# Kernel tuning notes

Measured on AMD Instinct MI355X. Metric: run time of the kernel, lower is better.

Reference implementation:

```python
import jax, jax.numpy as jnp
import numpy as np

NF = 64      # num_feat
NFR = 5      # num_frames
G = 8        # offset/deformable groups
CENTER = NFR // 2
K = 9        # 3x3 taps


def conv3x3(x, w, b):
    y = jax.lax.conv_general_dilated(x, w, (1, 1), 'SAME',
                                     dimension_numbers=('NCHW', 'OIHW', 'NCHW'))
    return y + b[None, :, None, None]


def mdcn(x, offsets, masks, w, b):
    # x: [B,C,H,W]; offsets: [B,2*G*K,H,W] (layout g,k,(y,x)); masks: [B,G*K,H,W]
    B, C, H, W = x.shape
    Cg = C // G
    off = offsets.reshape(B, G, K, 2, H, W)
    oy, ox = off[:, :, :, 0], off[:, :, :, 1]          # [B,G,K,H,W]
    m = masks.reshape(B, G, K, H, W)
    ky = jnp.repeat(jnp.arange(3), 3) - 1              # [K]
    kx = jnp.tile(jnp.arange(3), 3) - 1
    base_y = (ky[:, None, None] + jnp.arange(H)[None, :, None]).astype(x.dtype)  # [K,H,1]
    base_x = (kx[:, None, None] + jnp.arange(W)[None, None, :]).astype(x.dtype)  # [K,1,W]
    py = oy + base_y[None, None]                        # [B,G,K,H,W]
    px = ox + base_x[None, None]
    y0f = jnp.floor(py); x0f = jnp.floor(px)
    ty = py - y0f; tx = px - x0f
    y0 = y0f.astype(jnp.int32); x0 = x0f.astype(jnp.int32)
    xg = x.reshape(B, G, Cg, H * W)

    def gather(yi, xi):
        valid = (yi >= 0) & (yi < H) & (xi >= 0) & (xi < W)
        yc = jnp.clip(yi, 0, H - 1); xc = jnp.clip(xi, 0, W - 1)
        idx = (yc * W + xc).reshape(B, G, 1, K * H * W)
        idx = jnp.broadcast_to(idx, (B, G, Cg, K * H * W))
        v = jnp.take_along_axis(xg, idx, axis=3).reshape(B, G, Cg, K, H, W)
        return v * valid.reshape(B, G, 1, K, H, W)

    v00 = gather(y0, x0); v01 = gather(y0, x0 + 1)
    v10 = gather(y0 + 1, x0); v11 = gather(y0 + 1, x0 + 1)
    ty_ = ty[:, :, None]; tx_ = tx[:, :, None]          # [B,G,1,K,H,W]
    samp = (v00 * (1 - ty_) * (1 - tx_) + v01 * (1 - ty_) * tx_ +
            v10 * ty_ * (1 - tx_) + v11 * ty_ * tx_)
    samp = samp * m[:, :, None]                          # modulation
    wr = w.reshape(-1, G, Cg, K)                         # [Cout,G,Cg,K]
    out = jnp.einsum('bgckhw,ogck->bohw', samp, wr)
    return out + b[None, :, None, None]


def setup_inputs():
    key = jax.random.key(0)
    ks = jax.random.split(key, 16)
    def mk(k, shape, fan_in):
        return jax.random.normal(k, shape, jnp.float32) * (1.0 / np.sqrt(fan_in))
    B, H, W = 1, 160, 160
    return {
        'x':   jax.random.normal(ks[0], (B, NFR, 4, H, W), jnp.float32),
        'fw1': mk(ks[1], (NF, 4, 3, 3), 4 * 9),   'fb1': jnp.zeros((NF,), jnp.float32),
        'fw2': mk(ks[2], (NF, NF, 3, 3), NF * 9), 'fb2': jnp.zeros((NF,), jnp.float32),
        'fw3': mk(ks[3], (NF, NF, 3, 3), NF * 9), 'fb3': jnp.zeros((NF,), jnp.float32),
        'ow1': mk(ks[4], (NF, 2 * NF, 3, 3), 2 * NF * 9), 'ob1': jnp.zeros((NF,), jnp.float32),
        'ow2': mk(ks[5], (NF, NF, 3, 3), NF * 9),         'ob2': jnp.zeros((NF,), jnp.float32),
        'ow3': mk(ks[6], (G * 27, NF, 3, 3), NF * 9) * 0.1,
        'ob3': jnp.zeros((G * 27,), jnp.float32),
        'dw':  mk(ks[7], (NF, NF, 3, 3), NF * 9), 'db': jnp.zeros((NF,), jnp.float32),
    }


def reference(x, fw1, fb1, fw2, fb2, fw3, fb3, ow1, ob1, ow2, ob2, ow3, ob3, dw, db):
    B, N, C, H, W = x.shape
    f = x.reshape(B * N, C, H, W)
    f = jax.nn.relu(conv3x3(f, fw1, fb1))
    f = jax.nn.relu(conv3x3(f, fw2, fb2))
    f = jax.nn.relu(conv3x3(f, fw3, fb3))
    feats = f.reshape(B, N, NF, H, W)
    ref = feats[:, CENTER]                               # [B,NF,H,W]
    nc = np.array([i for i in range(N) if i != CENTER])
    curr = feats[:, nc].reshape(B * (N - 1), NF, H, W)
    ref_t = jnp.broadcast_to(ref[:, None], (B, N - 1, NF, H, W)).reshape(B * (N - 1), NF, H, W)
    cat = jnp.concatenate([ref_t, curr], axis=1)         # [B(N-1),2*NF,H,W]
    o = jax.nn.relu(conv3x3(cat, ow1, ob1))
    o = jax.nn.relu(conv3x3(o, ow2, ob2))
    raw = conv3x3(o, ow3, ob3)                           # [B(N-1),27G,H,W]
    offsets = raw[:, :G * 18]
    masks = jax.nn.sigmoid(raw[:, G * 18:])
    aligned = mdcn(curr, offsets, masks, dw, db)
    aligned = aligned.reshape(B, N - 1, NF, H, W)
    return jnp.concatenate([aligned[:, :CENTER], ref[:, None], aligned[:, CENTER:]], axis=1)
```

## Files before the change

### kernel.cpp

```cpp
#include <hip/hip_runtime.h>
#include <hip/hip_bf16.h>
#include <math.h>

#define HH 160
#define WW 160
#define HWsz (HH*WW)

typedef short bf16x8 __attribute__((ext_vector_type(8)));
typedef float f32x4  __attribute__((ext_vector_type(4)));

__device__ inline ushort f2bf(float f) {
    unsigned int u = __float_as_uint(f);
    unsigned int r = (u + 0x7FFFu + ((u >> 16) & 1u)) >> 16;
    return (ushort)r;
}

__device__ inline void unpk8(uint4 u, float* f) {
    f[0] = __uint_as_float(u.x << 16); f[1] = __uint_as_float(u.x & 0xFFFF0000u);
    f[2] = __uint_as_float(u.y << 16); f[3] = __uint_as_float(u.y & 0xFFFF0000u);
    f[4] = __uint_as_float(u.z << 16); f[5] = __uint_as_float(u.z & 0xFFFF0000u);
    f[6] = __uint_as_float(u.w << 16); f[7] = __uint_as_float(u.w & 0xFFFF0000u);
}

__global__ __launch_bounds__(256)
void pack_all(const float* __restrict__ fw2, const float* __restrict__ fw3,
              const float* __restrict__ ow1, const float* __restrict__ ow2,
              const float* __restrict__ ow3, const float* __restrict__ dw,
              ushort* __restrict__ w2p, ushort* __restrict__ w3p,
              ushort* __restrict__ o1p, ushort* __restrict__ o2p,
              ushort* __restrict__ o3p, ushort* __restrict__ wmp)
{
    const int seg = blockIdx.y;
    const int idx = blockIdx.x * 256 + threadIdx.x;

    if (seg == 5) {
        if (idx >= 18 * 4 * 64) return;
        const int lane = idx & 63;
        const int mt   = (idx >> 6) & 3;
        const int chunk = idx >> 8;
        const int o  = mt * 16 + (lane & 15);
        const int gk = chunk * 4 + (lane >> 4);
        const int g  = gk / 9, k = gk % 9;
        ushort v[8];
#pragma unroll
        for (int j = 0; j < 8; ++j)
            v[j] = f2bf(dw[((size_t)o * 64 + g * 8 + j) * 9 + k]);
        uint4 pk;
        pk.x = (unsigned)v[0] | ((unsigned)v[1] << 16);
        pk.y = (unsigned)v[2] | ((unsigned)v[3] << 16);
        pk.z = (unsigned)v[4] | ((unsigned)v[5] << 16);
        pk.w = (unsigned)v[6] | ((unsigned)v[7] << 16);
        *(uint4*)(wmp + (size_t)idx * 8) = pk;
        return;
    }

    const float* w; ushort* wp; int Cout, Cin, MT_TOT, CIC;
    switch (seg) {
        case 0: w = fw2; wp = w2p; Cout = 64;  Cin = 64;  MT_TOT = 4;  CIC = 2; break;
        case 1: w = fw3; wp = w3p; Cout = 64;  Cin = 64;  MT_TOT = 4;  CIC = 2; break;
        case 2: w = ow1; wp = o1p; Cout = 64;  Cin = 128; MT_TOT = 4;  CIC = 4; break;
        case 3: w = ow2; wp = o2p; Cout = 64;  Cin = 64;  MT_TOT = 4;  CIC = 2; break;
        default: w = ow3; wp = o3p; Cout = 216; Cin = 64; MT_TOT = 16; CIC = 2; break;
    }
    const int total = 9 * CIC * MT_TOT * 64;
    if (idx >= total) return;
    const int lane = idx & 63;
    int t = idx >> 6;
    const int mt  = t % MT_TOT; t /= MT_TOT;
    const int cic = t % CIC;    t /= CIC;
    const int tap = t;
    const int co  = mt * 16 + (lane & 15);
    const int ci0 = cic * 32 + (lane >> 4) * 8;
    ushort v[8];
#pragma unroll
    for (int j = 0; j < 8; ++j) {
        const int ci = ci0 + j;
        float f = 0.f;
        if (co < Cout && ci < Cin) f = w[((size_t)co * Cin + ci) * 9 + tap];
        v[j] = f2bf(f);
    }
    uint4 pk;
    pk.x = (unsigned)v[0] | ((unsigned)v[1] << 16);
    pk.y = (unsigned)v[2] | ((unsigned)v[3] << 16);
    pk.z = (unsigned)v[4] | ((unsigned)v[5] << 16);
    pk.w = (unsigned)v[6] | ((unsigned)v[7] << 16);
    *(uint4*)(wp + (size_t)idx * 8) = pk;
}

template<int CIC_TILE, int CI_STEPS, bool CONCAT, bool RELU, int OMODE>
__global__ __launch_bounds__(256, 3)
void mfma_conv(const ushort* __restrict__ in, const ushort* __restrict__ wp,
               const float* __restrict__ bias, void* __restrict__ outv,
               int Cout, int MT_TOT, int COG,
               float* __restrict__ outmain, ushort* __restrict__ ftsg)
{
    constexpr int ROWS = 8, HR = ROWS + 2, NT = 4;
    constexpr int C8   = CIC_TILE * 4;
    constexpr int CICT = CIC_TILE * CI_STEPS;
    constexpr int CIN  = CICT * 32;
    __shared__ uint4 s_in4[HR * 34 * C8];

    const int tid = threadIdx.x;
    const int lane = tid & 63, wid = tid >> 6;
    const int lane15 = lane & 15, lgrp = lane >> 4;
    const int bz = blockIdx.z;
    const int frame = bz / COG, cog = bz % COG;
    const int x0 = blockIdx.x * 32, y0 = blockIdx.y * ROWS;

    const ushort* src = nullptr; const ushort* srcRef = nullptr; const ushort* srcCur = nullptr;
    if (CONCAT) {
        const int fidx = (frame < 2) ? frame : frame + 1;
        srcRef = in + (size_t)2 * HWsz * 64;
        srcCur = in + (size_t)fidx * HWsz * 64;
    } else {
        src = in + (size_t)frame * HWsz * CIN;
    }

    f32x4 acc[4][NT];
#pragma unroll
    for (int m = 0; m < 4; ++m)
#pragma unroll
        for (int n = 0; n < NT; ++n) acc[m][n] = (f32x4){0.f, 0.f, 0.f, 0.f};

    const uint4* wp4 = (const uint4*)wp;
    const int wrow = wid * 2;
    const int mtg0 = cog * 4;

    for (int step = 0; step < CI_STEPS; ++step) {
        if (step) __syncthreads();
        for (int i = tid; i < HR * 34 * C8; i += 256) {
            const int ci8l = i & (C8 - 1);
            const int rem = i / C8;
            const int col = rem % 34, row = rem / 34;
            const int gy = y0 + row - 1, gx = x0 + col - 1;
            const int gci8 = step * C8 + ci8l;
            uint4 v = {0u, 0u, 0u, 0u};
            if (gy >= 0 && gy < HH && gx >= 0 && gx < WW) {
                if (CONCAT) {
                    const ushort* sp = (gci8 < 8) ? srcRef : srcCur;
                    v = *(const uint4*)(sp + (size_t)(gy * WW + gx) * 64 + (gci8 & 7) * 8);
                } else {
                    v = *(const uint4*)(src + (size_t)(gy * WW + gx) * CIN + gci8 * 8);
                }
            }
            s_in4[(row * 34 + col) * C8 + (ci8l ^ (col & 7))] = v;
        }
        __syncthreads();

#pragma unroll 3
        for (int tap = 0; tap < 9; ++tap) {
            const int dy  = tap / 3 - 1;
            const int dxp = tap % 3;
#pragma unroll
            for (int cic = 0; cic < CIC_TILE; ++cic) {
                const uint4* ap = wp4 +
                    ((size_t)(tap * CICT + step * CIC_TILE + cic) * MT_TOT + mtg0) * 64 + lane;
                bf16x8 a[4];
#pragma unroll
                for (int mt = 0; mt < 4; ++mt)
                    a[mt] = *(const bf16x8*)(ap + (size_t)mt * 64);
#pragma unroll
                for (int nt = 0; nt < NT; ++nt) {
                    const int row_l = wrow + (nt >> 1) + dy + 1;
                    const int col_l = (nt & 1) * 16 + lane15 + dxp;
                    const bf16x8 b = *(const bf16x8*)
                        &s_in4[(row_l * 34 + col_l) * C8 + ((cic * 4 + lgrp) ^ (col_l & 7))];
#pragma unroll
                    for (int mt = 0; mt < 4; ++mt)
                        acc[mt][nt] = __builtin_amdgcn_mfma_f32_16x16x32_bf16(a[mt], b, acc[mt][nt], 0, 0, 0);
                }
            }
        }
    }

#pragma unroll
    for (int mt = 0; mt < 4; ++mt) {
        const int co = cog * 64 + mt * 16 + lgrp * 4;
        if (co < Cout) {
            const float4 bs = *(const float4*)&bias[co];
#pragma unroll
            for (int nt = 0; nt < NT; ++nt) {
                const int yy = y0 + wrow + (nt >> 1);
                const int xx = x0 + (nt & 1) * 16 + lane15;
                const int hw = yy * WW + xx;
                f32x4 v = acc[mt][nt];
                v[0] += bs.x; v[1] += bs.y; v[2] += bs.z; v[3] += bs.w;
                if (RELU) {
                    v[0] = fmaxf(v[0], 0.f); v[1] = fmaxf(v[1], 0.f);
                    v[2] = fmaxf(v[2], 0.f); v[3] = fmaxf(v[3], 0.f);
                }
                if (OMODE <= 1) {
                    uint2 pk;
                    pk.x = (unsigned)f2bf(v[0]) | ((unsigned)f2bf(v[1]) << 16);
                    pk.y = (unsigned)f2bf(v[2]) | ((unsigned)f2bf(v[3]) << 16);
                    *(uint2*)((ushort*)outv + ((size_t)frame * HWsz + hw) * 64 + co) = pk;
                    if (OMODE == 1) {
                        if (frame == 2) {
#pragma unroll
                            for (int j = 0; j < 4; ++j)
                                outmain[((size_t)(128 + co + j)) * HWsz + hw] = v[j];
                        } else {
                            const int b = (frame < 2) ? frame : frame - 1;
                            *(uint2*)(ftsg + (((size_t)(b * 8 + (co >> 3)) * HWsz + hw) * 8 + (co & 7))) = pk;
                        }
                    }
                } else {
                    ushort* rawp = (ushort*)outv + (size_t)frame * 72 * HWsz * 4;
                    const ushort h0 = f2bf(v[0]), h1 = f2bf(v[1]);
                    const ushort h2 = f2bf(v[2]), h3 = f2bf(v[3]);
                    if (co < 144) {
                        *(unsigned*)(rawp + ((size_t)(co >> 1) * HWsz + hw) * 4) =
                            (unsigned)h0 | ((unsigned)h1 << 16);
                        *(unsigned*)(rawp + ((size_t)((co >> 1) + 1) * HWsz + hw) * 4) =
                            (unsigned)h2 | ((unsigned)h3 << 16);
                    } else {
                        const int gk0 = co - 144;
                        rawp[((size_t)(gk0 + 0) * HWsz + hw) * 4 + 2] = h0;
                        rawp[((size_t)(gk0 + 1) * HWsz + hw) * 4 + 2] = h1;
                        rawp[((size_t)(gk0 + 2) * HWsz + hw) * 4 + 2] = h2;
                        rawp[((size_t)(gk0 + 3) * HWsz + hw) * 4 + 2] = h3;
                    }
                }
            }
        }
    }
}

__global__ __launch_bounds__(256)
void conv1_kernel(const float* __restrict__ x, const float* __restrict__ w,
                  const float* __restrict__ b, ushort* __restrict__ out)
{
    const int fr = blockIdx.z;
    const int t = threadIdx.x;
    const int tx = t & 15, ty = t >> 4;
    const int x0 = blockIdx.x * 16, y0 = blockIdx.y * 16;

    __shared__ float s_x[4][18][18];
    __shared__ float s_w[36][64];
    __shared__ float s_b[64];

    for (int i = t; i < 4 * 18 * 18; i += 256) {
        const int ci = i / 324, rem = i % 324;
        const int yy = rem / 18, xx = rem % 18;
        const int gy = y0 + yy - 1, gx = x0 + xx - 1;
        float v = 0.f;
        if (gy >= 0 && gy < HH && gx >= 0 && gx < WW)
            v = x[((size_t)fr * 4 + ci) * HWsz + gy * WW + gx];
        s_x[ci][yy][xx] = v;
    }
    for (int i = t; i < 36 * 64; i += 256) {
        const int row = i / 64, o = i % 64;
        const int ci = row / 9, tap = row % 9;
        s_w[row][o] = w[((size_t)o * 4 + ci) * 9 + tap];
    }
    if (t < 64) s_b[t] = b[t];
    __syncthreads();

    float acc[64];
#pragma unroll
    for (int i = 0; i < 64; ++i) acc[i] = 0.f;

#pragma unroll
    for (int ci = 0; ci < 4; ++ci) {
#pragma unroll
        for (int tap = 0; tap < 9; ++tap) {
            const float v = s_x[ci][ty + tap / 3][tx + tap % 3];
            const float4* wr = (const float4*)&s_w[ci * 9 + tap][0];
#pragma unroll
            for (int o4 = 0; o4 < 16; ++o4) {
                const float4 wv = wr[o4];
                acc[o4 * 4 + 0] = fmaf(v, wv.x, acc[o4 * 4 + 0]);
                acc[o4 * 4 + 1] = fmaf(v, wv.y, acc[o4 * 4 + 1]);
                acc[o4 * 4 + 2] = fmaf(v, wv.z, acc[o4 * 4 + 2]);
                acc[o4 * 4 + 3] = fmaf(v, wv.w, acc[o4 * 4 + 3]);
            }
        }
    }

    ushort* ob = out + ((size_t)fr * HWsz + (y0 + ty) * WW + (x0 + tx)) * 64;
#pragma unroll
    for (int o8 = 0; o8 < 8; ++o8) {
        ushort v[8];
#pragma unroll
        for (int j = 0; j < 8; ++j)
            v[j] = f2bf(fmaxf(acc[o8 * 8 + j] + s_b[o8 * 8 + j], 0.f));
        uint4 pk;
        pk.x = (unsigned)v[0] | ((unsigned)v[1] << 16);
        pk.y = (unsigned)v[2] | ((unsigned)v[3] << 16);
        pk.z = (unsigned)v[4] | ((unsigned)v[5] << 16);
        pk.w = (unsigned)v[6] | ((unsigned)v[7] << 16);
        *(uint4*)(ob + o8 * 8) = pk;
    }
}

__global__ __launch_bounds__(256)
void mdcn_mfma(const ushort* __restrict__ ftsg, const ushort* __restrict__ rawpk,
               const ushort* __restrict__ wmp, const float* __restrict__ db,
               float* __restrict__ out)
{
    const int b    = blockIdx.z;
    const int fidx = (b < 2) ? b : b + 1;
    const int tid  = threadIdx.x;
    const int lane = tid & 63, wid = tid >> 6;
    const int lane15 = lane & 15, lgrp = lane >> 4;
    const int x = blockIdx.x * 16 + lane15;
    const int y = blockIdx.y * 4 + wid;
    const int hw = y * WW + x;

    const ushort* rawb = rawpk + (size_t)b * 72 * HWsz * 4;
    const uint4* wmp4 = (const uint4*)wmp;

    f32x4 acc[4];
#pragma unroll
    for (int m = 0; m < 4; ++m) acc[m] = (f32x4){0.f, 0.f, 0.f, 0.f};

#pragma unroll 2
    for (int chunk = 0; chunk < 18; ++chunk) {
        const int gk = chunk * 4 + lgrp;
        const int g  = gk / 9, k = gk - 9 * g;
        const int kyy = k / 3 - 1, kxx = k % 3 - 1;

        const uint2 rr = *(const uint2*)(rawb + ((size_t)gk * HWsz + hw) * 4);
        const float oy = __uint_as_float(rr.x << 16);
        const float ox = __uint_as_float(rr.x & 0xFFFF0000u);
        const float mraw = __uint_as_float(rr.y << 16);
        const float mv = 1.f / (1.f + __expf(-mraw));

        const float py = oy + (float)(y + kyy);
        const float px = ox + (float)(x + kxx);
        const float y0f = floorf(py), x0f = floorf(px);
        const float tyf = py - y0f, txf = px - x0f;
        const int y0 = (int)y0f, x0i = (int)x0f;
        const int y1 = y0 + 1, x1 = x0i + 1;
        const bool vy0 = (y0 >= 0) & (y0 < HH);
        const bool vy1 = (y1 >= 0) & (y1 < HH);
        const bool vx0 = (x0i >= 0) & (x0i < WW);
        const bool vx1 = (x1 >= 0) & (x1 < WW);
        const int yc0 = min(max(y0, 0), HH - 1), yc1 = min(max(y1, 0), HH - 1);
        const int xc0 = min(max(x0i, 0), WW - 1), xc1 = min(max(x1, 0), WW - 1);
        const float a0 = (1.f - tyf) * mv, a1 = tyf * mv;
        float w00 = a0 * (1.f - txf);
        float w01 = a0 * txf;
        float w10 = a1 * (1.f - txf);
        float w11 = a1 * txf;
        if (!(vy0 && vx0)) w00 = 0.f;
        if (!(vy0 && vx1)) w01 = 0.f;
        if (!(vy1 && vx0)) w10 = 0.f;
        if (!(vy1 && vx1)) w11 = 0.f;

        const ushort* pb = ftsg + (size_t)(b * 8 + g) * HWsz * 8;
        const uint4 u00 = *(const uint4*)(pb + (size_t)(yc0 * WW + xc0) * 8);
        const uint4 u01 = *(const uint4*)(pb + (size_t)(yc0 * WW + xc1) * 8);
        const uint4 u10 = *(const uint4*)(pb + (size_t)(yc1 * WW + xc0) * 8);
        const uint4 u11 = *(const uint4*)(pb + (size_t)(yc1 * WW + xc1) * 8);
        float f00[8], f01[8], f10[8], f11[8];
        unpk8(u00, f00); unpk8(u01, f01); unpk8(u10, f10); unpk8(u11, f11);

        float s[8];
#pragma unroll
        for (int c = 0; c < 8; ++c)
            s[c] = fmaf(w11, f11[c], fmaf(w10, f10[c],
                    fmaf(w01, f01[c], w00 * f00[c])));
        uint4 bpk;
        asm("v_cvt_pk_bf16_f32 %0, %1, %2" : "=v"(bpk.x) : "v"(s[0]), "v"(s[1]));
        asm("v_cvt_pk_bf16_f32 %0, %1, %2" : "=v"(bpk.y) : "v"(s[2]), "v"(s[3]));
        asm("v_cvt_pk_bf16_f32 %0, %1, %2" : "=v"(bpk.z) : "v"(s[4]), "v"(s[5]));
        asm("v_cvt_pk_bf16_f32 %0, %1, %2" : "=v"(bpk.w) : "v"(s[6]), "v"(s[7]));
        const bf16x8 bfrag = __builtin_bit_cast(bf16x8, bpk);

#pragma unroll
        for (int mt = 0; mt < 4; ++mt) {
            const bf16x8 a = *(const bf16x8*)&wmp4[(size_t)(chunk * 4 + mt) * 64 + lane];
            acc[mt] = __builtin_amdgcn_mfma_f32_16x16x32_bf16(a, bfrag, acc[mt], 0, 0, 0);
        }
    }

    float* ob = out + (size_t)fidx * 64 * HWsz + hw;
#pragma unroll
    for (int mt = 0; mt < 4; ++mt) {
        const int o0 = mt * 16 + lgrp * 4;
        const float4 bs = *(const float4*)&db[o0];
        ob[(size_t)(o0 + 0) * HWsz] = acc[mt][0] + bs.x;
        ob[(size_t)(o0 + 1) * HWsz] = acc[mt][1] + bs.y;
        ob[(size_t)(o0 + 2) * HWsz] = acc[mt][2] + bs.z;
        ob[(size_t)(o0 + 3) * HWsz] = acc[mt][3] + bs.w;
    }
}

extern "C" void kernel_launch(void* const* d_in, const int* in_sizes, int n_in,
                              void* d_out, int out_size, void* d_ws, size_t ws_size,
                              hipStream_t stream)
{
    const float* x   = (const float*)d_in[0];
    const float* fw1 = (const float*)d_in[1];
    const float* fb1 = (const float*)d_in[2];
    const float* fw2 = (const float*)d_in[3];
    const float* fb2 = (const float*)d_in[4];
    const float* fw3 = (const float*)d_in[5];
    const float* fb3 = (const float*)d_in[6];
    const float* ow1 = (const float*)d_in[7];
    const float* ob1 = (const float*)d_in[8];
    const float* ow2 = (const float*)d_in[9];
    const float* ob2 = (const float*)d_in[10];
    const float* ow3 = (const float*)d_in[11];
    const float* ob3 = (const float*)d_in[12];
    const float* dw  = (const float*)d_in[13];
    const float* db  = (const float*)d_in[14];
    float* out = (float*)d_out;

    ushort* buf1 = (ushort*)d_ws;
    ushort* buf2 = buf1 + (size_t)5 * HWsz * 64;
    ushort* fts  = buf2 + (size_t)5 * HWsz * 64;
    ushort* ftsg = fts + (size_t)5 * HWsz * 64;
    ushort* raw  = ftsg + (size_t)4 * 8 * HWsz * 8;
    ushort* w2p  = raw + (size_t)4 * 72 * HWsz * 4;
    ushort* w3p  = w2p + 36864;
    ushort* o1p  = w3p + 36864;
    ushort* o2p  = o1p + 73728;
    ushort* o3p  = o2p + 36864;
    ushort* wmp  = o3p + 147456;

    const dim3 blk(256);

    pack_all<<<dim3(72, 6), blk, 0, stream>>>(fw2, fw3, ow1, ow2, ow3, dw,
                                              w2p, w3p, o1p, o2p, o3p, wmp);

    conv1_kernel<<<dim3(10, 10, 5), blk, 0, stream>>>(x, fw1, fb1, buf1);
    mfma_conv<2, 1, false, true, 0><<<dim3(5, 20, 5), blk, 0, stream>>>(
        buf1, w2p, fb2, buf2, 64, 4, 1, nullptr, nullptr);
    mfma_conv<2, 1, false, true, 1><<<dim3(5, 20, 5), blk, 0, stream>>>(
        buf2, w3p, fb3, fts, 64, 4, 1, out, ftsg);

    mfma_conv<2, 2, true, true, 0><<<dim3(5, 20, 4), blk, 0, stream>>>(
        fts, o1p, ob1, buf1, 64, 4, 1, nullptr, nullptr);
    mfma_conv<2, 1, false, true, 0><<<dim3(5, 20, 4), blk, 0, stream>>>(
        buf1, o2p, ob2, buf2, 64, 4, 1, nullptr, nullptr);
    mfma_conv<2, 1, false, false, 3><<<dim3(5, 20, 16), blk, 0, stream>>>(
        buf2, o3p, ob3, raw, 216, 16, 4, nullptr, nullptr);

    mdcn_mfma<<<dim3(10, 40, 4), blk, 0, stream>>>(ftsg, raw, wmp, db, out);
}
```

Baseline: 216.6 us.

## Stage conv weights in shared memory and split offset/mask buffers

The MFMA conv kernel now cooperatively loads each half of the per-tap weight fragments into LDS and reads A operands from there, instead of every wave fetching them directly from global memory. This adds extra barriers and LDS footprint, and lowers the occupancy hint from 3 to 2 blocks per SM. The raw offset/mask output is also split into a packed 32-bit offset plane and a separate 16-bit mask plane. This replaces the padded 4-ushort interleave, shrinking the bytes the last conv writes and the deformable kernel reads.

After: 197.8 us. 8.7% less time.

```diff
diff --git a/kernel.cpp b/kernel.cpp
--- a/kernel.cpp
+++ b/kernel.cpp
@@ -87,18 +87,19 @@
     *(uint4*)(wp + (size_t)idx * 8) = pk;
 }
 
-template<int CIC_TILE, int CI_STEPS, bool CONCAT, bool RELU, int OMODE>
-__global__ __launch_bounds__(256, 3)
+template<int CI_STEPS, bool CONCAT, bool RELU, int OMODE>
+__global__ __launch_bounds__(256, 2)
 void mfma_conv(const ushort* __restrict__ in, const ushort* __restrict__ wp,
                const float* __restrict__ bias, void* __restrict__ outv,
                int Cout, int MT_TOT, int COG,
-               float* __restrict__ outmain, ushort* __restrict__ ftsg)
+               float* __restrict__ outmain, ushort* __restrict__ aux)
 {
     constexpr int ROWS = 8, HR = ROWS + 2, NT = 4;
-    constexpr int C8   = CIC_TILE * 4;
-    constexpr int CICT = CIC_TILE * CI_STEPS;
+    constexpr int C8   = 8;
+    constexpr int CICT = 2 * CI_STEPS;
     constexpr int CIN  = CICT * 32;
     __shared__ uint4 s_in4[HR * 34 * C8];
+    __shared__ uint4 s_a4[9 * 4 * 64];
 
     const int tid = threadIdx.x;
     const int lane = tid & 63, wid = tid >> 6;
@@ -126,39 +127,49 @@
     const int wrow = wid * 2;
     const int mtg0 = cog * 4;
 
+#pragma unroll
     for (int step = 0; step < CI_STEPS; ++step) {
-        if (step) __syncthreads();
-        for (int i = tid; i < HR * 34 * C8; i += 256) {
-            const int ci8l = i & (C8 - 1);
-            const int rem = i / C8;
-            const int col = rem % 34, row = rem / 34;
-            const int gy = y0 + row - 1, gx = x0 + col - 1;
-            const int gci8 = step * C8 + ci8l;
-            uint4 v = {0u, 0u, 0u, 0u};
-            if (gy >= 0 && gy < HH && gx >= 0 && gx < WW) {
-                if (CONCAT) {
-                    const ushort* sp = (gci8 < 8) ? srcRef : srcCur;
-                    v = *(const uint4*)(sp + (size_t)(gy * WW + gx) * 64 + (gci8 & 7) * 8);
-                } else {
-                    v = *(const uint4*)(src + (size_t)(gy * WW + gx) * CIN + gci8 * 8);
+#pragma unroll
+        for (int half = 0; half < 2; ++half) {
+            if (half == 0) {
+                for (int i = tid; i < HR * 34 * C8; i += 256) {
+                    const int ci8l = i & (C8 - 1);
+                    const int rem = i / C8;
+                    const int col = rem % 34, row = rem / 34;
+                    const int gy = y0 + row - 1, gx = x0 + col - 1;
+                    const int gci8 = step * C8 + ci8l;
+                    uint4 v = {0u, 0u, 0u, 0u};
+                    if (gy >= 0 && gy < HH && gx >= 0 && gx < WW) {
+                        if (CONCAT) {
+                            const ushort* sp = (gci8 < 8) ? srcRef : srcCur;
+                            v = *(const uint4*)(sp + (size_t)(gy * WW + gx) * 64 + (gci8 & 7) * 8);
+                        } else {
+                            v = *(const uint4*)(src + (size_t)(gy * WW + gx) * CIN + gci8 * 8);
+                        }
+                    }
+                    s_in4[(row * 34 + col) * C8 + (ci8l ^ (col & 7))] = v;
                 }
             }
-            s_in4[(row * 34 + col) * C8 + (ci8l ^ (col & 7))] = v;
-        }
-        __syncthreads();
-
-#pragma unroll 3
-        for (int tap = 0; tap < 9; ++tap) {
-            const int dy  = tap / 3 - 1;
-            const int dxp = tap % 3;
-#pragma unroll
-            for (int cic = 0; cic < CIC_TILE; ++cic) {
-                const uint4* ap = wp4 +
-                    ((size_t)(tap * CICT + step * CIC_TILE + cic) * MT_TOT + mtg0) * 64 + lane;
+#pragma unroll
+            for (int it = 0; it < 9; ++it) {
+                const int i = tid + it * 256;
+                const int ln = i & 63, mt = (i >> 6) & 3, kkl = i >> 8;
+                const int kkg = half * 9 + kkl;
+                const int tap = kkg >> 1, cic = kkg & 1;
+                s_a4[i] = wp4[((size_t)(tap * CICT + step * 2 + cic) * MT_TOT + mtg0 + mt) * 64 + ln];
+            }
+            __syncthreads();
+
+#pragma unroll
+            for (int kkl = 0; kkl < 9; ++kkl) {
+                const int kkg = half * 9 + kkl;
+                const int tap = kkg >> 1, cic = kkg & 1;
+                const int dy  = tap / 3 - 1;
+                const int dxp = tap % 3;
                 bf16x8 a[4];
 #pragma unroll
                 for (int mt = 0; mt < 4; ++mt)
-                    a[mt] = *(const bf16x8*)(ap + (size_t)mt * 64);
+                    a[mt] = *(const bf16x8*)&s_a4[(kkl * 4 + mt) * 64 + lane];
 #pragma unroll
                 for (int nt = 0; nt < NT; ++nt) {
                     const int row_l = wrow + (nt >> 1) + dy + 1;
@@ -170,6 +181,7 @@
                         acc[mt][nt] = __builtin_amdgcn_mfma_f32_16x16x32_bf16(a[mt], b, acc[mt][nt], 0, 0, 0);
                 }
             }
+            __syncthreads();
         }
     }
 
@@ -201,24 +213,23 @@
                                 outmain[((size_t)(128 + co + j)) * HWsz + hw] = v[j];
                         } else {
                             const int b = (frame < 2) ? frame : frame - 1;
-                            *(uint2*)(ftsg + (((size_t)(b * 8 + (co >> 3)) * HWsz + hw) * 8 + (co & 7))) = pk;
+                            *(uint2*)(aux + (((size_t)(b * 8 + (co >> 3)) * HWsz + hw) * 8 + (co & 7))) = pk;
                         }
                     }
                 } else {
-                    ushort* rawp = (ushort*)outv + (size_t)frame * 72 * HWsz * 4;
                     const ushort h0 = f2bf(v[0]), h1 = f2bf(v[1]);
                     const ushort h2 = f2bf(v[2]), h3 = f2bf(v[3]);
                     if (co < 144) {
-                        *(unsigned*)(rawp + ((size_t)(co >> 1) * HWsz + hw) * 4) =
-                            (unsigned)h0 | ((unsigned)h1 << 16);
-                        *(unsigned*)(rawp + ((size_t)((co >> 1) + 1) * HWsz + hw) * 4) =
-                            (unsigned)h2 | ((unsigned)h3 << 16);
+                        unsigned* roff = (unsigned*)outv + (size_t)frame * 72 * HWsz;
+                        roff[(size_t)(co >> 1) * HWsz + hw]       = (unsigned)h0 | ((unsigned)h1 << 16);
+                        roff[(size_t)((co >> 1) + 1) * HWsz + hw] = (unsigned)h2 | ((unsigned)h3 << 16);
                     } else {
+                        ushort* rmsk = aux + (size_t)frame * 72 * HWsz;
                         const int gk0 = co - 144;
-                        rawp[((size_t)(gk0 + 0) * HWsz + hw) * 4 + 2] = h0;
-                        rawp[((size_t)(gk0 + 1) * HWsz + hw) * 4 + 2] = h1;
-                        rawp[((size_t)(gk0 + 2) * HWsz + hw) * 4 + 2] = h2;
-                        rawp[((size_t)(gk0 + 3) * HWsz + hw) * 4 + 2] = h3;
+                        rmsk[(size_t)(gk0 + 0) * HWsz + hw] = h0;
+                        rmsk[(size_t)(gk0 + 1) * HWsz + hw] = h1;
+                        rmsk[(size_t)(gk0 + 2) * HWsz + hw] = h2;
+                        rmsk[(size_t)(gk0 + 3) * HWsz + hw] = h3;
                     }
                 }
             }
@@ -294,7 +305,8 @@
 }
 
 __global__ __launch_bounds__(256)
-void mdcn_mfma(const ushort* __restrict__ ftsg, const ushort* __restrict__ rawpk,
+void mdcn_mfma(const ushort* __restrict__ ftsg, const unsigned* __restrict__ roffg,
+               const ushort* __restrict__ rmskg,
                const ushort* __restrict__ wmp, const float* __restrict__ db,
                float* __restrict__ out)
 {
@@ -307,7 +319,8 @@
     const int y = blockIdx.y * 4 + wid;
     const int hw = y * WW + x;
 
-    const ushort* rawb = rawpk + (size_t)b * 72 * HWsz * 4;
+    const unsigned* roff = roffg + (size_t)b * 72 * HWsz;
+    const ushort*   rmsk = rmskg + (size_t)b * 72 * HWsz;
     const uint4* wmp4 = (const uint4*)wmp;
 
     f32x4 acc[4];
@@ -320,10 +333,11 @@
         const int g  = gk / 9, k = gk - 9 * g;
         const int kyy = k / 3 - 1, kxx = k % 3 - 1;
 
-        const uint2 rr = *(const uint2*)(rawb + ((size_t)gk * HWsz + hw) * 4);
-        const float oy = __uint_as_float(rr.x << 16);
-        const float ox = __uint_as_float(rr.x & 0xFFFF0000u);
-        const float mraw = __uint_as_float(rr.y << 16);
+        const unsigned op = roff[(size_t)gk * HWsz + hw];
+        const ushort   mu = rmsk[(size_t)gk * HWsz + hw];
+        const float oy = __uint_as_float(op << 16);
+        const float ox = __uint_as_float(op & 0xFFFF0000u);
+        const float mraw = __uint_as_float((unsigned)mu << 16);
         const float mv = 1.f / (1.f + __expf(-mraw));
 
         const float py = oy + (float)(y + kyy);
@@ -412,8 +426,9 @@
     ushort* buf2 = buf1 + (size_t)5 * HWsz * 64;
     ushort* fts  = buf2 + (size_t)5 * HWsz * 64;
     ushort* ftsg = fts + (size_t)5 * HWsz * 64;
-    ushort* raw  = ftsg + (size_t)4 * 8 * HWsz * 8;
-    ushort* w2p  = raw + (size_t)4 * 72 * HWsz * 4;
+    unsigned* roff = (unsigned*)(ftsg + (size_t)4 * 8 * HWsz * 8);
+    ushort* rmsk = (ushort*)(roff + (size_t)4 * 72 * HWsz);
+    ushort* w2p  = rmsk + (size_t)4 * 72 * HWsz;
     ushort* w3p  = w2p + 36864;
     ushort* o1p  = w3p + 36864;
     ushort* o2p  = o1p + 73728;
@@ -426,17 +441,17 @@
                                               w2p, w3p, o1p, o2p, o3p, wmp);
 
     conv1_kernel<<<dim3(10, 10, 5), blk, 0, stream>>>(x, fw1, fb1, buf1);
-    mfma_conv<2, 1, false, true, 0><<<dim3(5, 20, 5), blk, 0, stream>>>(
+    mfma_conv<1, false, true, 0><<<dim3(5, 20, 5), blk, 0, stream>>>(
         buf1, w2p, fb2, buf2, 64, 4, 1, nullptr, nullptr);
-    mfma_conv<2, 1, false, true, 1><<<dim3(5, 20, 5), blk, 0, stream>>>(
+    mfma_conv<1, false, true, 1><<<dim3(5, 20, 5), blk, 0, stream>>>(
         buf2, w3p, fb3, fts, 64, 4, 1, out, ftsg);
 
-    mfma_conv<2, 2, true, true, 0><<<dim3(5, 20, 4), blk, 0, stream>>>(
+    mfma_conv<2, true, true, 0><<<dim3(5, 20, 4), blk, 0, stream>>>(
         fts, o1p, ob1, buf1, 64, 4, 1, nullptr, nullptr);
-    mfma_conv<2, 1, false, true, 0><<<dim3(5, 20, 4), blk, 0, stream>>>(
+    mfma_conv<1, false, true, 0><<<dim3(5, 20, 4), blk, 0, stream>>>(
         buf1, o2p, ob2, buf2, 64, 4, 1, nullptr, nullptr);
-    mfma_conv<2, 1, false, false, 3><<<dim3(5, 20, 16), blk, 0, stream>>>(
-        buf2, o3p, ob3, raw, 216, 16, 4, nullptr, nullptr);
-
-    mdcn_mfma<<<dim3(10, 40, 4), blk, 0, stream>>>(ftsg, raw, wmp, db, out);
-}
+    mfma_conv<1, false, false, 3><<<dim3(5, 20, 16), blk, 0, stream>>>(
+        buf2, o3p, ob3, roff, 216, 16, 4, nullptr, rmsk);
+
+    mdcn_mfma<<<dim3(10, 40, 4), blk, 0, stream>>>(ftsg, roff, rmsk, wmp, db, out);
+}
```
